# Performance work log

Measured on AMD Instinct MI355X. Metric: run time of the kernel, lower is better.

Reference implementation:

```python
import jax, jax.numpy as jnp
import numpy as np

N_NODES = 100000
N_EDGES = 1600000
NFEAT = 128
NCLASS = 40


def setup_inputs() -> dict:
    key = jax.random.key(0)
    k1, k2, k3 = jax.random.split(key, 3)
    x = jax.random.normal(k1, (N_NODES, NFEAT), dtype=jnp.float32)
    edge_index = jax.random.randint(k2, (2, N_EDGES), 0, N_NODES, dtype=jnp.int64)
    W = jax.random.normal(k3, (NFEAT, NCLASS), dtype=jnp.float32) * (1.0 / np.sqrt(NFEAT))
    b = jnp.zeros((NCLASS,), dtype=jnp.float32)
    return {"x": x, "edge_index": edge_index, "W": W, "b": b, "k": 3}


def reference(x, edge_index, W, b, k):
    N = x.shape[0]
    # gcn_norm with add_self_loops=True (PyG SGConv default)
    loop = jnp.arange(N, dtype=edge_index.dtype)
    row = jnp.concatenate([edge_index[0], loop])  # source nodes (x_j)
    col = jnp.concatenate([edge_index[1], loop])  # target nodes (aggregation index)
    deg = jax.ops.segment_sum(jnp.ones_like(col, dtype=x.dtype), col, num_segments=N)
    dis = jnp.where(deg > 0, jax.lax.rsqrt(deg), 0.0)  # deg^{-1/2}, inf -> 0
    norm = (dis[row] * dis[col])[:, None]  # [E+N, 1]
    # k hops of sparse propagation: out[col] += norm * x[row]
    for _ in range(k):
        x = jax.ops.segment_sum(norm * x[row], col, num_segments=N)
    # final linear projection
    return x @ W + b
```

## Files before the change

### kernel.cpp

```cpp
#include <hip/hip_runtime.h>

#define N_NODES 100000
#define N_EDGES 1600000
#define NFEAT 128
#define NCLASS 40
#define SCAN_BLK 98


__global__ void cnt_zero(int* __restrict__ cnt) {
    int i = blockIdx.x * blockDim.x + threadIdx.x;
    if (i < N_NODES) cnt[i] = 0;
}

__global__ void cnt_count(const int* __restrict__ col, int* __restrict__ cnt) {
    int e = blockIdx.x * blockDim.x + threadIdx.x;
    if (e < N_EDGES) atomicAdd(&cnt[col[e]], 1);
}


__global__ void scan_partial(const int* __restrict__ cnt, int* __restrict__ bsum) {
    __shared__ int red[256];
    int blk = blockIdx.x, tid = threadIdx.x;
    int base = blk * 1024 + tid * 4;
    int s = 0;
    if (base + 3 < N_NODES) {
        int4 v = *reinterpret_cast<const int4*>(cnt + base);
        s = v.x + v.y + v.z + v.w;
    } else {
        for (int i = 0; i < 4; ++i) if (base + i < N_NODES) s += cnt[base + i];
    }
    red[tid] = s;
    __syncthreads();
    for (int o = 128; o > 0; o >>= 1) {
        if (tid < o) red[tid] += red[tid + o];
        __syncthreads();
    }
    if (tid == 0) bsum[blk] = red[0];
}

__global__ void scan_base(int* __restrict__ bsum, int* __restrict__ rowptr) {
    __shared__ int s[128];
    int tid = threadIdx.x;
    s[tid] = (tid < SCAN_BLK) ? bsum[tid] : 0;
    __syncthreads();
    for (int o = 1; o < 128; o <<= 1) {
        int v = s[tid];
        int a = (tid >= o) ? s[tid - o] : 0;
        __syncthreads();
        s[tid] = v + a;
        __syncthreads();
    }
    if (tid < SCAN_BLK) bsum[tid] = (tid == 0) ? 0 : s[tid - 1];
    if (tid == 0) rowptr[N_NODES] = s[SCAN_BLK - 1];
}

__global__ void scan_write(const int* __restrict__ cnt, const int* __restrict__ bsum,
                           int* __restrict__ rowptr, int* __restrict__ cursor,
                           float* __restrict__ dis) {
    __shared__ int psum[256];
    int blk = blockIdx.x, tid = threadIdx.x;
    int base = blk * 1024 + tid * 4;
    int c0 = 0, c1 = 0, c2 = 0, c3 = 0;
    if (base + 3 < N_NODES) {
        int4 v = *reinterpret_cast<const int4*>(cnt + base);
        c0 = v.x; c1 = v.y; c2 = v.z; c3 = v.w;
    } else {
        if (base < N_NODES)     c0 = cnt[base];
        if (base + 1 < N_NODES) c1 = cnt[base + 1];
        if (base + 2 < N_NODES) c2 = cnt[base + 2];
        if (base + 3 < N_NODES) c3 = cnt[base + 3];
    }
    int s = c0 + c1 + c2 + c3;
    psum[tid] = s;
    __syncthreads();
    for (int o = 1; o < 256; o <<= 1) {
        int v = psum[tid];
        int a = (tid >= o) ? psum[tid - o] : 0;
        __syncthreads();
        psum[tid] = v + a;
        __syncthreads();
    }
    int ex = psum[tid] - s + bsum[blk];
    if (base + 3 < N_NODES) {
        int4 rp = make_int4(ex, ex + c0, ex + c0 + c1, ex + c0 + c1 + c2);
        *reinterpret_cast<int4*>(rowptr + base) = rp;
        *reinterpret_cast<int4*>(cursor + base) = rp;
        float4 dv = make_float4(rsqrtf((float)c0 + 1.0f), rsqrtf((float)c1 + 1.0f),
                                rsqrtf((float)c2 + 1.0f), rsqrtf((float)c3 + 1.0f));
        *reinterpret_cast<float4*>(dis + base) = dv;
    } else {
        int r = ex;
        if (base < N_NODES)     { rowptr[base] = r;     cursor[base] = r;     dis[base] = rsqrtf((float)c0 + 1.0f);     r += c0; }
        if (base + 1 < N_NODES) { rowptr[base + 1] = r; cursor[base + 1] = r; dis[base + 1] = rsqrtf((float)c1 + 1.0f); r += c1; }
        if (base + 2 < N_NODES) { rowptr[base + 2] = r; cursor[base + 2] = r; dis[base + 2] = rsqrtf((float)c2 + 1.0f); r += c2; }
        if (base + 3 < N_NODES) { rowptr[base + 3] = r; cursor[base + 3] = r; dis[base + 3] = rsqrtf((float)c3 + 1.0f); }
    }
}


__global__ void scatter_csr(const int* __restrict__ row, const int* __restrict__ col,
                            int* __restrict__ cursor, int* __restrict__ csr) {
    int e = blockIdx.x * blockDim.x + threadIdx.x;
    if (e >= N_EDGES) return;
    int c = col[e];
    int slot = atomicAdd(&cursor[c], 1);
    csr[slot] = row[e];
}


__global__ void gemm_xw(const float* __restrict__ x, const float* __restrict__ W,
                        const float* __restrict__ dis, float* __restrict__ z) {
    int n = blockIdx.x * blockDim.x + threadIdx.x;
    if (n >= N_NODES) return;
    const float4* xr = reinterpret_cast<const float4*>(x + (size_t)n * NFEAT);
    float acc[NCLASS];
#pragma unroll
    for (int c = 0; c < NCLASS; ++c) acc[c] = 0.0f;
    for (int fb = 0; fb < NFEAT / 4; ++fb) {
        float4 xv = xr[fb];
#pragma unroll
        for (int j = 0; j < 4; ++j) {
            float xs = (&xv.x)[j];
            const float* wrow = W + (fb * 4 + j) * NCLASS;
#pragma unroll
            for (int c = 0; c < NCLASS; ++c) acc[c] += xs * wrow[c];
        }
    }
    float d = dis[n];
    float4* zr = reinterpret_cast<float4*>(z + (size_t)n * NCLASS);
#pragma unroll
    for (int cb = 0; cb < NCLASS / 4; ++cb)
        zr[cb] = make_float4(d * acc[cb * 4], d * acc[cb * 4 + 1],
                             d * acc[cb * 4 + 2], d * acc[cb * 4 + 3]);
}


template <int FINAL>
__global__ void hop_pull(const int* __restrict__ rowptr, const int* __restrict__ csr,
                         const float* __restrict__ dis, const float* __restrict__ zin,
                         const float* __restrict__ b, float* __restrict__ zout) {
    int wid = (blockIdx.x * blockDim.x + threadIdx.x) >> 6;
    int lane = threadIdx.x & 63;
    if (wid >= N_NODES) return;
    int beg = rowptr[wid];
    int end = rowptr[wid + 1];
    float acc = 0.0f;
    if (lane < NCLASS) acc = zin[wid * NCLASS + lane];
    int k = beg;
    int n4 = beg + ((end - beg) & ~3);
    for (; k < n4; k += 4) {
        int p0 = csr[k], p1 = csr[k + 1], p2 = csr[k + 2], p3 = csr[k + 3];
        if (lane < NCLASS) {
            float g0 = zin[p0 * NCLASS + lane];
            float g1 = zin[p1 * NCLASS + lane];
            float g2 = zin[p2 * NCLASS + lane];
            float g3 = zin[p3 * NCLASS + lane];
            acc += g0 + g1 + g2 + g3;
        }
    }
    for (; k < end; ++k) {
        int p = csr[k];
        if (lane < NCLASS) acc += zin[p * NCLASS + lane];
    }
    if (lane < NCLASS) {
        float d = dis[wid];
        float r;
        if (FINAL) r = d * acc + b[lane];
        else       r = d * d * acc;
        zout[wid * NCLASS + lane] = r;
    }
}


extern "C" void kernel_launch(void* const* d_in, const int* in_sizes, int n_in,
                              void* d_out, int out_size, void* d_ws, size_t ws_size,
                              hipStream_t stream) {
    const float* x = (const float*)d_in[0];
    const int* ei = (const int*)d_in[1];
    const float* W = (const float*)d_in[2];
    const float* b = (const float*)d_in[3];

    const int* row = ei;
    const int* col = ei + N_EDGES;

    char* ws = (char*)d_ws;
    size_t off = 0;
    auto alloc = [&](size_t bytes) { void* p = ws + off; off += (bytes + 255) & ~(size_t)255; return p; };
    int*   cnt    = (int*)  alloc((size_t)N_NODES * 4);
    float* dis    = (float*)alloc((size_t)N_NODES * 4);
    int*   rowptr = (int*)  alloc((size_t)(N_NODES + 1) * 4);
    int*   cursor = (int*)  alloc((size_t)N_NODES * 4);
    int*   bsum   = (int*)  alloc(128 * 4);
    int*   csr    = (int*)  alloc((size_t)N_EDGES * 4);
    float* buf0   = (float*)alloc((size_t)N_NODES * NCLASS * 4);
    float* outf   = (float*)d_out;

    const int B = 256;
    cnt_zero<<<(N_NODES + B - 1) / B, B, 0, stream>>>(cnt);
    cnt_count<<<(N_EDGES + B - 1) / B, B, 0, stream>>>(col, cnt);
    scan_partial<<<SCAN_BLK, 256, 0, stream>>>(cnt, bsum);
    scan_base<<<1, 128, 0, stream>>>(bsum, rowptr);
    scan_write<<<SCAN_BLK, 256, 0, stream>>>(cnt, bsum, rowptr, cursor, dis);
    scatter_csr<<<(N_EDGES + B - 1) / B, B, 0, stream>>>(row, col, cursor, csr);

    gemm_xw<<<(N_NODES + B - 1) / B, B, 0, stream>>>(x, W, dis, buf0);

    int grid_hop = (int)(((size_t)N_NODES * 64 + B - 1) / B);
    hop_pull<0><<<grid_hop, B, 0, stream>>>(rowptr, csr, dis, buf0, nullptr, outf);
    hop_pull<0><<<grid_hop, B, 0, stream>>>(rowptr, csr, dis, outf, nullptr, buf0);
    hop_pull<1><<<grid_hop, B, 0, stream>>>(rowptr, csr, dis, buf0, b, outf);
}
```

Baseline: 529.0 us.

## Build CSR via two-pass bucketed radix scatter instead of global atomics

```diff
diff --git a/kernel.cpp b/kernel.cpp
--- a/kernel.cpp
+++ b/kernel.cpp
@@ -5,6 +5,13 @@
 #define NFEAT 128
 #define NCLASS 40
 #define SCAN_BLK 98
+
+#define BKT_SHIFT 9
+#define BKT_COLS 512
+#define N_BKT 196
+#define P1_CHUNK 4096
+#define P1_GRID ((N_EDGES + P1_CHUNK - 1) / P1_CHUNK)
+#define P2_CAP 12288
 
 
 __global__ void cnt_zero(int* __restrict__ cnt) {
@@ -55,8 +62,7 @@
 }
 
 __global__ void scan_write(const int* __restrict__ cnt, const int* __restrict__ bsum,
-                           int* __restrict__ rowptr, int* __restrict__ cursor,
-                           float* __restrict__ dis) {
+                           int* __restrict__ rowptr, float* __restrict__ dis) {
     __shared__ int psum[256];
     int blk = blockIdx.x, tid = threadIdx.x;
     int base = blk * 1024 + tid * 4;
@@ -84,27 +90,104 @@
     if (base + 3 < N_NODES) {
         int4 rp = make_int4(ex, ex + c0, ex + c0 + c1, ex + c0 + c1 + c2);
         *reinterpret_cast<int4*>(rowptr + base) = rp;
-        *reinterpret_cast<int4*>(cursor + base) = rp;
         float4 dv = make_float4(rsqrtf((float)c0 + 1.0f), rsqrtf((float)c1 + 1.0f),
                                 rsqrtf((float)c2 + 1.0f), rsqrtf((float)c3 + 1.0f));
         *reinterpret_cast<float4*>(dis + base) = dv;
     } else {
         int r = ex;
-        if (base < N_NODES)     { rowptr[base] = r;     cursor[base] = r;     dis[base] = rsqrtf((float)c0 + 1.0f);     r += c0; }
-        if (base + 1 < N_NODES) { rowptr[base + 1] = r; cursor[base + 1] = r; dis[base + 1] = rsqrtf((float)c1 + 1.0f); r += c1; }
-        if (base + 2 < N_NODES) { rowptr[base + 2] = r; cursor[base + 2] = r; dis[base + 2] = rsqrtf((float)c2 + 1.0f); r += c2; }
-        if (base + 3 < N_NODES) { rowptr[base + 3] = r; cursor[base + 3] = r; dis[base + 3] = rsqrtf((float)c3 + 1.0f); }
-    }
-}
-
-
-__global__ void scatter_csr(const int* __restrict__ row, const int* __restrict__ col,
-                            int* __restrict__ cursor, int* __restrict__ csr) {
-    int e = blockIdx.x * blockDim.x + threadIdx.x;
-    if (e >= N_EDGES) return;
-    int c = col[e];
-    int slot = atomicAdd(&cursor[c], 1);
-    csr[slot] = row[e];
+        if (base < N_NODES)     { rowptr[base] = r;     dis[base] = rsqrtf((float)c0 + 1.0f);     r += c0; }
+        if (base + 1 < N_NODES) { rowptr[base + 1] = r; dis[base + 1] = rsqrtf((float)c1 + 1.0f); r += c1; }
+        if (base + 2 < N_NODES) { rowptr[base + 2] = r; dis[base + 2] = rsqrtf((float)c2 + 1.0f); r += c2; }
+        if (base + 3 < N_NODES) { rowptr[base + 3] = r; dis[base + 3] = rsqrtf((float)c3 + 1.0f); }
+    }
+}
+
+
+__global__ void bcur_init(const int* __restrict__ rowptr, int* __restrict__ bcur) {
+    int t = threadIdx.x;
+    if (t < N_BKT) bcur[t] = rowptr[t * BKT_COLS];
+}
+
+
+__global__ __launch_bounds__(256) void bucket_scatter(const int* __restrict__ row,
+                                                      const int* __restrict__ col,
+                                                      int* __restrict__ bcur,
+                                                      int2* __restrict__ pairs) {
+    __shared__ int hist[256];
+    __shared__ int pref[256];
+    __shared__ int excl[256];
+    __shared__ int gb[N_BKT];
+    __shared__ int2 out[P1_CHUNK];
+    __shared__ int dst[P1_CHUNK];
+    int tid = threadIdx.x;
+    int e0 = blockIdx.x * P1_CHUNK;
+    hist[tid] = 0;
+    __syncthreads();
+    int myr[16], myc[16];
+    bool val[16];
+#pragma unroll
+    for (int j = 0; j < 16; ++j) {
+        int e = e0 + j * 256 + tid;
+        val[j] = e < N_EDGES;
+        if (val[j]) {
+            myc[j] = col[e];
+            myr[j] = row[e];
+            atomicAdd(&hist[myc[j] >> BKT_SHIFT], 1);
+        }
+    }
+    __syncthreads();
+    int v = hist[tid];
+    if (tid < N_BKT && v > 0) gb[tid] = atomicAdd(&bcur[tid], v);
+    else if (tid < N_BKT) gb[tid] = 0;
+    pref[tid] = v;
+    __syncthreads();
+    for (int o = 1; o < 256; o <<= 1) {
+        int vv = pref[tid];
+        int a = (tid >= o) ? pref[tid - o] : 0;
+        __syncthreads();
+        pref[tid] = vv + a;
+        __syncthreads();
+    }
+    excl[tid] = pref[tid] - v;
+    __syncthreads();
+    hist[tid] = excl[tid];
+    __syncthreads();
+#pragma unroll
+    for (int j = 0; j < 16; ++j) {
+        if (val[j]) {
+            int b = myc[j] >> BKT_SHIFT;
+            int l = atomicAdd(&hist[b], 1);
+            out[l] = make_int2(myr[j], myc[j]);
+            dst[l] = gb[b] + (l - excl[b]);
+        }
+    }
+    __syncthreads();
+    int tot = pref[255];
+    for (int i = tid; i < tot; i += 256) pairs[dst[i]] = out[i];
+}
+
+
+__global__ __launch_bounds__(256) void csr_build(const int* __restrict__ rowptr,
+                                                 const int2* __restrict__ pairs,
+                                                 int* __restrict__ csr) {
+    __shared__ int cur[BKT_COLS];
+    __shared__ int stage[P2_CAP];
+    int b = blockIdx.x, tid = threadIdx.x;
+    int lo = b * BKT_COLS;
+    int hi = lo + BKT_COLS; if (hi > N_NODES) hi = N_NODES;
+    int base = rowptr[lo];
+    int cnt = rowptr[hi] - base;
+    for (int c = tid; c < hi - lo; c += 256) cur[c] = rowptr[lo + c] - base;
+    __syncthreads();
+    for (int i = tid; i < cnt; i += 256) {
+        int2 p = pairs[base + i];
+        int s = atomicAdd(&cur[p.y - lo], 1);
+        if (s < P2_CAP) stage[s] = p.x;
+        else csr[base + s] = p.x;
+    }
+    __syncthreads();
+    int lim = cnt < P2_CAP ? cnt : P2_CAP;
+    for (int i = tid; i < lim; i += 256) csr[base + i] = stage[i];
 }
 
 
@@ -189,8 +272,9 @@
     int*   cnt    = (int*)  alloc((size_t)N_NODES * 4);
     float* dis    = (float*)alloc((size_t)N_NODES * 4);
     int*   rowptr = (int*)  alloc((size_t)(N_NODES + 1) * 4);
-    int*   cursor = (int*)  alloc((size_t)N_NODES * 4);
     int*   bsum   = (int*)  alloc(128 * 4);
+    int*   bcur   = (int*)  alloc(256 * 4);
+    int2*  pairs  = (int2*) alloc((size_t)N_EDGES * 8);
     int*   csr    = (int*)  alloc((size_t)N_EDGES * 4);
     float* buf0   = (float*)alloc((size_t)N_NODES * NCLASS * 4);
     float* outf   = (float*)d_out;
@@ -200,8 +284,10 @@
     cnt_count<<<(N_EDGES + B - 1) / B, B, 0, stream>>>(col, cnt);
     scan_partial<<<SCAN_BLK, 256, 0, stream>>>(cnt, bsum);
     scan_base<<<1, 128, 0, stream>>>(bsum, rowptr);
-    scan_write<<<SCAN_BLK, 256, 0, stream>>>(cnt, bsum, rowptr, cursor, dis);
-    scatter_csr<<<(N_EDGES + B - 1) / B, B, 0, stream>>>(row, col, cursor, csr);
+    scan_write<<<SCAN_BLK, 256, 0, stream>>>(cnt, bsum, rowptr, dis);
+    bcur_init<<<1, 256, 0, stream>>>(rowptr, bcur);
+    bucket_scatter<<<P1_GRID, 256, 0, stream>>>(row, col, bcur, pairs);
+    csr_build<<<N_BKT, 256, 0, stream>>>(rowptr, pairs, csr);
 
     gemm_xw<<<(N_NODES + B - 1) / B, B, 0, stream>>>(x, W, dis, buf0);
 
```

After: 449.8 us. -15.0%, faster.
